# Kernel optimization log

Measured on AMD Instinct MI355X. Metric: run time of the kernel, lower is better.

The kernel has to match this reference:

```python
import math
import jax, jax.numpy as jnp
import numpy as np

S, D = 4096, 2048
H, DH = 16, 128
ROPE_BASE = 10000.0


def _rotate_half(x):
    # x: [..., dh]; pairs (x1, x2) -> (-x2, x1), interleaved
    shp = x.shape
    x = x.reshape(*shp[:-1], shp[-1] // 2, 2)
    x1, x2 = x[..., 0], x[..., 1]
    return jnp.stack((-x2, x1), axis=-1).reshape(shp)


def _rope_cos_sin(seq_len, dh):
    inv_freq = 1.0 / (ROPE_BASE ** (jnp.arange(0, dh, 2, dtype=jnp.float32) / dh))
    t = jnp.arange(seq_len, dtype=jnp.float32)
    freqs = jnp.einsum('i,j->ij', t, inv_freq)  # [S, dh/2]
    cos = jnp.repeat(jnp.cos(freqs), 2, axis=-1)  # [S, dh]
    sin = jnp.repeat(jnp.sin(freqs), 2, axis=-1)
    return cos, sin


def setup_inputs() -> dict:
    key = jax.random.key(0)
    kx, kq, kk, kv, ko = jax.random.split(key, 5)
    scale_in = 1.0 / math.sqrt(D)
    scale_hd = 1.0 / math.sqrt(H * DH)
    return {
        'x': jax.random.normal(kx, (S, D), dtype=jnp.float32),
        'mask': jnp.tril(jnp.ones((S, S), dtype=bool)),  # causal
        'wq': jax.random.normal(kq, (H * DH, D), dtype=jnp.float32) * scale_in,
        'wk': jax.random.normal(kk, (H * DH, D), dtype=jnp.float32) * scale_in,
        'wv': jax.random.normal(kv, (H * DH, D), dtype=jnp.float32) * scale_in,
        'wo': jax.random.normal(ko, (D, H * DH), dtype=jnp.float32) * scale_hd,
    }


def reference(x, mask, wq, wk, wv, wo):
    s = x.shape[0]
    # QKV projections (Linear: y = W @ x per token) -> [h, S, dh]
    q = (x @ wq.T).reshape(s, H, DH).transpose(1, 0, 2)
    k = (x @ wk.T).reshape(s, H, DH).transpose(1, 0, 2)
    v = (x @ wv.T).reshape(s, H, DH).transpose(1, 0, 2)
    # RoPE
    cos, sin = _rope_cos_sin(s, DH)  # [S, dh] each
    q = q * cos[None] + _rotate_half(q) * sin[None]
    k = k * cos[None] + _rotate_half(k) * sin[None]
    # Attention
    sim = jnp.einsum('hid,hjd->hij', q, k) / math.sqrt(DH)  # [h, S, S]
    sim = jnp.where(mask[None], sim, -jnp.inf)
    attn = jax.nn.softmax(sim, axis=-1)
    out = jnp.einsum('hij,hjd->ihd', attn, v).reshape(s, H * DH)
    return out @ wo.T
```

## Files before the change

kernel.cpp:

```cpp
#include <hip/hip_runtime.h>
#include <stdint.h>

#define S_LEN 4096
#define D_MODEL 2048
#define NH 16
#define DH 128

typedef short s16x8 __attribute__((ext_vector_type(8)));
typedef short s16x2 __attribute__((ext_vector_type(2)));
typedef unsigned short u16;
typedef unsigned short u16x4 __attribute__((ext_vector_type(4)));
typedef float f32x4 __attribute__((ext_vector_type(4)));

__device__ __forceinline__ u16 f2bf(float f) {
  union { float f; uint32_t u; } v; v.f = f;
  uint32_t u = v.u;
  u += 0x7FFFu + ((u >> 16) & 1u);
  return (u16)(u >> 16);
}

__device__ __forceinline__ float bf2f(u16 b) {
  union { uint32_t u; float f; } v; v.u = ((uint32_t)b) << 16;
  return v.f;
}

__device__ __forceinline__ void async_copy16(const u16* g, u16* l) {
  __builtin_amdgcn_global_load_lds(
      (const __attribute__((address_space(1))) unsigned int*)g,
      (__attribute__((address_space(3))) unsigned int*)l, 16, 0, 0);
}

__global__ void cast_kernel(const float4* __restrict__ src, u16* __restrict__ dst, int n4) {
  int i = blockIdx.x * blockDim.x + threadIdx.x;
  if (i >= n4) return;
  float4 v = src[i];
  u16x4 o;
  o[0] = f2bf(v.x); o[1] = f2bf(v.y); o[2] = f2bf(v.z); o[3] = f2bf(v.w);
  *(u16x4*)(dst + (size_t)i * 4) = o;
}

__global__ void cast4_kernel(const float4* __restrict__ s0, const float4* __restrict__ s1,
                             const float4* __restrict__ s2, const float4* __restrict__ s3,
                             u16* __restrict__ d0, u16* __restrict__ d1,
                             u16* __restrict__ d2, u16* __restrict__ d3) {
  int b = blockIdx.x;
  int which = b >> 12;
  const float4* src = which == 0 ? s0 : which == 1 ? s1 : which == 2 ? s2 : s3;
  u16* dst = which == 0 ? d0 : which == 1 ? d1 : which == 2 ? d2 : d3;
  int i = (b & 4095) * blockDim.x + threadIdx.x;
  float4 v = src[i];
  u16x4 o;
  o[0] = f2bf(v.x); o[1] = f2bf(v.y); o[2] = f2bf(v.z); o[3] = f2bf(v.w);
  *(u16x4*)(dst + (size_t)i * 4) = o;
}

__global__ void rope_table(float* __restrict__ ctab, float* __restrict__ stab) {
  int idx = blockIdx.x * blockDim.x + threadIdx.x;
  int t = idx >> 6, p = idx & 63;
  float invf = powf(10000.0f, -(float)p / 64.0f);
  float th = (float)t * invf;
  ctab[idx] = cosf(th);
  stab[idx] = sinf(th);
}

__global__ __launch_bounds__(256) void gemm_qkv(
    const u16* __restrict__ A,
    const u16* __restrict__ wqb, const u16* __restrict__ wkb, const u16* __restrict__ wvb,
    u16* __restrict__ qh, u16* __restrict__ kh, u16* __restrict__ vh,
    const float* __restrict__ ctab, const float* __restrict__ stab)
{
  __shared__ __align__(16) u16 la[128 * 64];
  __shared__ __align__(16) u16 lb[128 * 64];
  const int tid = threadIdx.x;
  const int w = tid >> 6, lane = tid & 63, quad = lane >> 4, l16 = lane & 15;
  const int wm = (w & 1) << 6, wn = (w >> 1) << 6;
  const int m0 = blockIdx.x << 7;
  const int n0g = blockIdx.y << 7;
  const int which = n0g >> 11;
  const int n0 = n0g & 2047;
  const u16* B = which == 0 ? wqb : which == 1 ? wkb : wvb;
  u16* outp = which == 0 ? qh : which == 1 ? kh : vh;
  const int K = D_MODEL;

  f32x4 zero = {0.f, 0.f, 0.f, 0.f};
  f32x4 acc[4][4];
#pragma unroll
  for (int i = 0; i < 4; ++i)
#pragma unroll
    for (int j = 0; j < 4; ++j) acc[i][j] = zero;

  for (int k0 = 0; k0 < K; k0 += 64) {
    __syncthreads();
#pragma unroll
    for (int rnd = 0; rnd < 4; ++rnd) {
      int c = rnd * 256 + w * 64 + lane;
      int r = c >> 3, cc = c & 7;
      int gcol = ((cc ^ (r & 7)) << 3);
      int base = (rnd * 256 + w * 64) << 3;
      async_copy16(A + (size_t)(m0 + r) * K + k0 + gcol, la + base);
      async_copy16(B + (size_t)(n0 + r) * K + k0 + gcol, lb + base);
    }
    __syncthreads();
#pragma unroll
    for (int ks = 0; ks < 2; ++ks) {
      s16x8 af[4], bfr[4];
#pragma unroll
      for (int t = 0; t < 4; ++t) {
        int rowa = wm + (t << 4) + l16;
        af[t] = *(const s16x8*)(la + (rowa << 6) + ((((ks << 2) + quad) ^ (rowa & 7)) << 3));
        int rowb = wn + (t << 4) + l16;
        bfr[t] = *(const s16x8*)(lb + (rowb << 6) + ((((ks << 2) + quad) ^ (rowb & 7)) << 3));
      }
#pragma unroll
      for (int mt = 0; mt < 4; ++mt)
#pragma unroll
        for (int nt = 0; nt < 4; ++nt)
          acc[mt][nt] = __builtin_amdgcn_mfma_f32_16x16x32_bf16(af[mt], bfr[nt], acc[mt][nt], 0, 0, 0);
    }
  }

#pragma unroll
  for (int mt = 0; mt < 4; ++mt) {
    int rowg = m0 + wm + (mt << 4) + (quad << 2);
#pragma unroll
    for (int nt = 0; nt < 4; ++nt) {
      int cl = n0 + wn + (nt << 4) + l16;
      int hh = cl >> 7, dd = cl & 127;
      int p = dd >> 1;
      f32x4 v = acc[mt][nt];
#pragma unroll
      for (int r = 0; r < 4; ++r) {
        float val = v[r];
        if (which < 2) {
          float partner = __shfl_xor(val, 1);
          float c = ctab[(size_t)(rowg + r) * 64 + p];
          float s = stab[(size_t)(rowg + r) * 64 + p];
          val = (dd & 1) ? fmaf(val, c, partner * s) : fmaf(val, c, -partner * s);
        }
        outp[((size_t)hh * S_LEN + (rowg + r)) * DH + dd] = f2bf(val);
      }
    }
  }
}

__global__ __launch_bounds__(256) void gemm_bf16(
    const u16* __restrict__ A, const u16* __restrict__ B,
    float* __restrict__ outF, int M, int N, int K)
{
  __shared__ __align__(16) u16 la[128 * 64];
  __shared__ __align__(16) u16 lb[128 * 64];
  const int tid = threadIdx.x;
  const int w = tid >> 6, lane = tid & 63, quad = lane >> 4, l16 = lane & 15;
  const int wm = (w & 1) << 6, wn = (w >> 1) << 6;
  const int m0 = blockIdx.x << 7, n0 = blockIdx.y << 7;

  f32x4 zero = {0.f, 0.f, 0.f, 0.f};
  f32x4 acc[4][4];
#pragma unroll
  for (int i = 0; i < 4; ++i)
#pragma unroll
    for (int j = 0; j < 4; ++j) acc[i][j] = zero;

  for (int k0 = 0; k0 < K; k0 += 64) {
    __syncthreads();
#pragma unroll
    for (int rnd = 0; rnd < 4; ++rnd) {
      int c = rnd * 256 + w * 64 + lane;
      int r = c >> 3, cc = c & 7;
      int gcol = ((cc ^ (r & 7)) << 3);
      int base = (rnd * 256 + w * 64) << 3;
      async_copy16(A + (size_t)(m0 + r) * K + k0 + gcol, la + base);
      async_copy16(B + (size_t)(n0 + r) * K + k0 + gcol, lb + base);
    }
    __syncthreads();
#pragma unroll
    for (int ks = 0; ks < 2; ++ks) {
      s16x8 af[4], bfr[4];
#pragma unroll
      for (int t = 0; t < 4; ++t) {
        int rowa = wm + (t << 4) + l16;
        af[t] = *(const s16x8*)(la + (rowa << 6) + ((((ks << 2) + quad) ^ (rowa & 7)) << 3));
        int rowb = wn + (t << 4) + l16;
        bfr[t] = *(const s16x8*)(lb + (rowb << 6) + ((((ks << 2) + quad) ^ (rowb & 7)) << 3));
      }
#pragma unroll
      for (int mt = 0; mt < 4; ++mt)
#pragma unroll
        for (int nt = 0; nt < 4; ++nt)
          acc[mt][nt] = __builtin_amdgcn_mfma_f32_16x16x32_bf16(af[mt], bfr[nt], acc[mt][nt], 0, 0, 0);
    }
  }

#pragma unroll
  for (int mt = 0; mt < 4; ++mt) {
    int rowg = m0 + wm + (mt << 4) + (quad << 2);
#pragma unroll
    for (int nt = 0; nt < 4; ++nt) {
      int col = n0 + wn + (nt << 4) + l16;
      f32x4 v = acc[mt][nt];
#pragma unroll
      for (int r = 0; r < 4; ++r) outF[(size_t)(rowg + r) * N + col] = v[r];
    }
  }
}

__global__ __launch_bounds__(512) void attn_kernel(
    const u16* __restrict__ Q, const u16* __restrict__ Kb,
    const u16* __restrict__ V,
    u16* __restrict__ U0, u16* __restrict__ U1, float* __restrict__ lbuf)
{
  __shared__ __align__(16) u16 lk[64 * 128];
  __shared__ __align__(16) u16 lvt[128 * 64];

  const int tid = threadIdx.x;
  const int w = tid >> 6, lane = tid & 63, quad = lane >> 4, l16 = lane & 15;
  const int h = blockIdx.y;
  const int bx = blockIdx.x;

  const u16* Qh = Q + (size_t)h * S_LEN * DH;
  const u16* Kh = Kb + (size_t)h * S_LEN * DH;
  const u16* Vh = V + (size_t)h * S_LEN * DH;

  const float scale = 0.08838834764831845f;
  const s16x8 vones = {0x3F80, 0x3F80, 0x3F80, 0x3F80, 0x3F80, 0x3F80, 0x3F80, 0x3F80};
  f32x4 zero = {0.f, 0.f, 0.f, 0.f};

  for (int seg = 0; seg < 2; ++seg) {
    const int qt = seg ? bx : (31 - bx);
    const int jlo = seg ? (qt + 1) : 0;
    const int jhi = seg ? (2 * qt + 2) : (qt + 1);
    const int i0 = qt << 7;
    const int iw = i0 + (w << 4);

    s16x8 qf[4];
#pragma unroll
    for (int ks = 0; ks < 4; ++ks)
      qf[ks] = *(const s16x8*)(Qh + (size_t)(iw + l16) * DH + ks * 32 + quad * 8);

    f32x4 accO[8];
#pragma unroll
    for (int dt = 0; dt < 8; ++dt) accO[dt] = zero;
    f32x4 accL = zero;

    for (int jt = jlo; jt < jhi; ++jt) {
      const int j0 = jt << 6;
      __syncthreads();
#pragma unroll
      for (int rnd = 0; rnd < 2; ++rnd) {
        int c = rnd * 512 + tid;
        int r = c >> 4, cc = c & 15;
        int gcol = ((cc ^ (r & 15)) << 3);
        async_copy16(Kh + (size_t)(j0 + r) * DH + gcol, lk + ((rnd * 512 + w * 64) << 3));
      }
      {
        int u = tid & 31;
        int c8 = tid >> 5;
        int r0 = u << 1;
        s16x8 v0 = *(const s16x8*)(Vh + (size_t)(j0 + r0) * DH + (c8 << 3));
        s16x8 v1 = *(const s16x8*)(Vh + (size_t)(j0 + r0 + 1) * DH + (c8 << 3));
        int cc = r0 >> 3;
#pragma unroll
        for (int e = 0; e < 8; ++e) {
          int d = (c8 << 3) + e;
          int off = (d << 6) + ((cc ^ (d & 7)) << 3) + (r0 & 7);
          s16x2 pr = {v0[e], v1[e]};
          *(s16x2*)(lvt + off) = pr;
        }
      }
      __syncthreads();

      f32x4 sa[4];
#pragma unroll
      for (int nt = 0; nt < 4; ++nt) sa[nt] = zero;
#pragma unroll
      for (int ks = 0; ks < 4; ++ks) {
#pragma unroll
        for (int nt = 0; nt < 4; ++nt) {
          int row = (nt << 4) + l16;
          s16x8 kf = *(const s16x8*)(lk + (row << 7) + ((((ks << 2) + quad) ^ (row & 15)) << 3));
          sa[nt] = __builtin_amdgcn_mfma_f32_16x16x32_bf16(qf[ks], kf, sa[nt], 0, 0, 0);
        }
      }

      __syncthreads();

      const bool maskt = (j0 + 63 > iw);
      u16* lpw = lk + (w << 10);
#pragma unroll
      for (int nt = 0; nt < 4; ++nt) {
        int col = (nt << 4) + l16;
        int j = j0 + col;
        int ccp = col >> 3;
#pragma unroll
        for (int r = 0; r < 4; ++r) {
          float raw = sa[nt][r];
          if (maskt) {
            int i = iw + (quad << 2) + r;
            if (j > i) raw = -1.0e30f;
          }
          float p = __expf(fmaf(raw, scale, -8.0f));
          union { float f; uint32_t u; } pv; pv.f = p;
          int m = (quad << 2) + r;
          lpw[(m << 6) + ((ccp ^ (m & 7)) << 3) + (col & 7)] = (u16)(pv.u >> 16);
        }
      }
      asm volatile("s_waitcnt lgkmcnt(0)" ::: "memory");
      s16x8 pf[2];
#pragma unroll
      for (int kp = 0; kp < 2; ++kp)
        pf[kp] = *(const s16x8*)(lpw + (l16 << 6) + ((((kp << 2) + quad) ^ (l16 & 7)) << 3));

      accL = __builtin_amdgcn_mfma_f32_16x16x32_bf16(pf[0], vones, accL, 0, 0, 0);
      accL = __builtin_amdgcn_mfma_f32_16x16x32_bf16(pf[1], vones, accL, 0, 0, 0);

#pragma unroll
      for (int dt = 0; dt < 8; ++dt) {
#pragma unroll
        for (int kp = 0; kp < 2; ++kp) {
          int row = (dt << 4) + l16;
          s16x8 vf = *(const s16x8*)(lvt + (row << 6) + ((((kp << 2) + quad) ^ (row & 7)) << 3));
          accO[dt] = __builtin_amdgcn_mfma_f32_16x16x32_bf16(pf[kp], vf, accO[dt], 0, 0, 0);
        }
      }
    }

    u16* Useg = seg ? U1 : U0;
    float* ls = lbuf + (size_t)seg * NH * S_LEN + (size_t)h * S_LEN;
#pragma unroll
    for (int r = 0; r < 4; ++r) {
      float lr = accL[r];
      float inv = lr > 0.f ? 1.0f / lr : 0.f;
      int srow = iw + (quad << 2) + r;
#pragma unroll
      for (int dt = 0; dt < 8; ++dt)
        Useg[((size_t)h * S_LEN + srow) * DH + (dt << 4) + l16] = f2bf(accO[dt][r] * inv);
      if (l16 == 0) ls[srow] = lr;
    }
  }
}

__global__ void combine_kernel(const u16* __restrict__ U0, const u16* __restrict__ U1,
                               const float* __restrict__ lbuf, u16* __restrict__ ob)
{
  int t = blockIdx.x * 256 + threadIdx.x;
  int d8 = t & 15;
  int h = (t >> 4) & 15;
  int s = t >> 8;
  float l0 = lbuf[(size_t)h * S_LEN + s];
  float l1 = lbuf[(size_t)(NH * S_LEN) + (size_t)h * S_LEN + s];
  float inv = 1.0f / (l0 + l1);
  float w0 = l0 * inv, w1 = l1 * inv;
  size_t base = ((size_t)h * S_LEN + s) * DH + d8 * 8;
  s16x8 u0 = *(const s16x8*)(U0 + base);
  s16x8 u1 = *(const s16x8*)(U1 + base);
  u16 o[8];
#pragma unroll
  for (int e = 0; e < 8; ++e)
    o[e] = f2bf(w0 * bf2f((u16)u0[e]) + w1 * bf2f((u16)u1[e]));
  *(s16x8*)(ob + ((size_t)s * D_MODEL + h * DH + d8 * 8)) = *(s16x8*)o;
}

extern "C" void kernel_launch(void* const* d_in, const int* in_sizes, int n_in,
                              void* d_out, int out_size, void* d_ws, size_t ws_size,
                              hipStream_t stream) {
  const float* x  = (const float*)d_in[0];
  const float* wq = (const float*)d_in[2];
  const float* wk = (const float*)d_in[3];
  const float* wv = (const float*)d_in[4];
  const float* wo = (const float*)d_in[5];
  float* out = (float*)d_out;

  char* ws = (char*)d_ws;
  u16* xb  = (u16*)(ws);
  u16* wqb = (u16*)(ws + (16ull << 20));
  u16* wkb = (u16*)(ws + (24ull << 20));
  u16* wvb = (u16*)(ws + (32ull << 20));
  u16* wob = (u16*)(ws + (40ull << 20));
  u16* qh  = (u16*)(ws + (48ull << 20));
  u16* kh  = (u16*)(ws + (64ull << 20));
  u16* vh  = (u16*)(ws + (80ull << 20));
  float* ctab = (float*)(ws + (96ull << 20));
  float* stab = (float*)(ws + (97ull << 20));
  u16* U0 = (u16*)(ws);
  u16* U1 = (u16*)(ws + (16ull << 20));
  float* lbuf = (float*)(ws + (32ull << 20));
  u16* ob = qh;

  const int nx4 = S_LEN * D_MODEL / 4;
  cast_kernel<<<nx4 / 256, 256, 0, stream>>>((const float4*)x, xb, nx4);
  cast4_kernel<<<4 * 4096, 256, 0, stream>>>(
      (const float4*)wq, (const float4*)wk, (const float4*)wv, (const float4*)wo,
      wqb, wkb, wvb, wob);
  rope_table<<<(S_LEN * 64) / 256, 256, 0, stream>>>(ctab, stab);

  gemm_qkv<<<dim3(S_LEN / 128, 3 * D_MODEL / 128), 256, 0, stream>>>(
      xb, wqb, wkb, wvb, qh, kh, vh, ctab, stab);

  attn_kernel<<<dim3(32, NH), 512, 0, stream>>>(qh, kh, vh, U0, U1, lbuf);
  combine_kernel<<<S_LEN * NH * 16 / 256, 256, 0, stream>>>(U0, U1, lbuf, ob);

  gemm_bf16<<<dim3(S_LEN / 128, D_MODEL / 128), 256, 0, stream>>>(
      ob, wob, out, S_LEN, D_MODEL, D_MODEL);
}
```

Baseline: 526.5 us.

## Double-buffer K/V tiles in attention kernel and prefetch next tile during compute

Splits the K and transposed-V shared tiles into two buffers and gives P its own shared region. The next tile's K is issued as an async copy and its V loaded into registers while the current tile's QK and PV MFMAs run, and the V transpose store goes into the alternate buffer. This cuts the per-iteration barriers from three to one. It also wraps the MFMA sections in s_setprio. The cost is more LDS per block (about 80KB) and more registers, which can lower occupancy.

```diff
diff --git a/kernel.cpp b/kernel.cpp
--- a/kernel.cpp
+++ b/kernel.cpp
@@ -209,8 +209,9 @@
     const u16* __restrict__ V,
     u16* __restrict__ U0, u16* __restrict__ U1, float* __restrict__ lbuf)
 {
-  __shared__ __align__(16) u16 lk[64 * 128];
-  __shared__ __align__(16) u16 lvt[128 * 64];
+  __shared__ __align__(16) u16 lk[2][64 * 128];
+  __shared__ __align__(16) u16 lvt[2][128 * 64];
+  __shared__ __align__(16) u16 lp[8 * 1024];
 
   const int tid = threadIdx.x;
   const int w = tid >> 6, lane = tid & 63, quad = lane >> 4, l16 = lane & 15;
@@ -224,6 +225,7 @@
   const float scale = 0.08838834764831845f;
   const s16x8 vones = {0x3F80, 0x3F80, 0x3F80, 0x3F80, 0x3F80, 0x3F80, 0x3F80, 0x3F80};
   f32x4 zero = {0.f, 0.f, 0.f, 0.f};
+  u16* lpw = lp + (w << 10);
 
   for (int seg = 0; seg < 2; ++seg) {
     const int qt = seg ? bx : (31 - bx);
@@ -242,50 +244,67 @@
     for (int dt = 0; dt < 8; ++dt) accO[dt] = zero;
     f32x4 accL = zero;
 
-    for (int jt = jlo; jt < jhi; ++jt) {
-      const int j0 = jt << 6;
-      __syncthreads();
+    {
+      const int j0 = jlo << 6;
+      int u = tid & 31, c8 = tid >> 5, r0 = u << 1;
+      s16x8 v0 = *(const s16x8*)(Vh + (size_t)(j0 + r0) * DH + (c8 << 3));
+      s16x8 v1 = *(const s16x8*)(Vh + (size_t)(j0 + r0 + 1) * DH + (c8 << 3));
 #pragma unroll
       for (int rnd = 0; rnd < 2; ++rnd) {
         int c = rnd * 512 + tid;
         int r = c >> 4, cc = c & 15;
         int gcol = ((cc ^ (r & 15)) << 3);
-        async_copy16(Kh + (size_t)(j0 + r) * DH + gcol, lk + ((rnd * 512 + w * 64) << 3));
-      }
-      {
-        int u = tid & 31;
-        int c8 = tid >> 5;
-        int r0 = u << 1;
-        s16x8 v0 = *(const s16x8*)(Vh + (size_t)(j0 + r0) * DH + (c8 << 3));
-        s16x8 v1 = *(const s16x8*)(Vh + (size_t)(j0 + r0 + 1) * DH + (c8 << 3));
-        int cc = r0 >> 3;
-#pragma unroll
-        for (int e = 0; e < 8; ++e) {
-          int d = (c8 << 3) + e;
-          int off = (d << 6) + ((cc ^ (d & 7)) << 3) + (r0 & 7);
-          s16x2 pr = {v0[e], v1[e]};
-          *(s16x2*)(lvt + off) = pr;
-        }
-      }
-      __syncthreads();
-
+        async_copy16(Kh + (size_t)(j0 + r) * DH + gcol, lk[0] + ((rnd * 512 + w * 64) << 3));
+      }
+      int cc = r0 >> 3;
+#pragma unroll
+      for (int e = 0; e < 8; ++e) {
+        int d = (c8 << 3) + e;
+        int off = (d << 6) + ((cc ^ (d & 7)) << 3) + (r0 & 7);
+        s16x2 pr = {v0[e], v1[e]};
+        *(s16x2*)(lvt[0] + off) = pr;
+      }
+    }
+    __syncthreads();
+
+    int cur = 0;
+    for (int jt = jlo; jt < jhi; ++jt) {
+      const int j0 = jt << 6;
+      const bool has_next = (jt + 1) < jhi;
+
+      s16x8 nv0, nv1;
+      if (has_next) {
+        const int nj0 = (jt + 1) << 6;
+        int u = tid & 31, c8 = tid >> 5, r0 = u << 1;
+        nv0 = *(const s16x8*)(Vh + (size_t)(nj0 + r0) * DH + (c8 << 3));
+        nv1 = *(const s16x8*)(Vh + (size_t)(nj0 + r0 + 1) * DH + (c8 << 3));
+#pragma unroll
+        for (int rnd = 0; rnd < 2; ++rnd) {
+          int c = rnd * 512 + tid;
+          int r = c >> 4, cc = c & 15;
+          int gcol = ((cc ^ (r & 15)) << 3);
+          async_copy16(Kh + (size_t)(nj0 + r) * DH + gcol,
+                       lk[cur ^ 1] + ((rnd * 512 + w * 64) << 3));
+        }
+      }
+
+      const u16* lkc = lk[cur];
       f32x4 sa[4];
 #pragma unroll
       for (int nt = 0; nt < 4; ++nt) sa[nt] = zero;
+      __builtin_amdgcn_s_setprio(1);
 #pragma unroll
       for (int ks = 0; ks < 4; ++ks) {
 #pragma unroll
         for (int nt = 0; nt < 4; ++nt) {
           int row = (nt << 4) + l16;
-          s16x8 kf = *(const s16x8*)(lk + (row << 7) + ((((ks << 2) + quad) ^ (row & 15)) << 3));
+          s16x8 kf = *(const s16x8*)(lkc + (row << 7) + ((((ks << 2) + quad) ^ (row & 15)) << 3));
           sa[nt] = __builtin_amdgcn_mfma_f32_16x16x32_bf16(qf[ks], kf, sa[nt], 0, 0, 0);
         }
       }
-
-      __syncthreads();
+      __builtin_amdgcn_s_setprio(0);
 
       const bool maskt = (j0 + 63 > iw);
-      u16* lpw = lk + (w << 10);
 #pragma unroll
       for (int nt = 0; nt < 4; ++nt) {
         int col = (nt << 4) + l16;
@@ -310,18 +329,36 @@
       for (int kp = 0; kp < 2; ++kp)
         pf[kp] = *(const s16x8*)(lpw + (l16 << 6) + ((((kp << 2) + quad) ^ (l16 & 7)) << 3));
 
+      if (has_next) {
+        int u = tid & 31, c8 = tid >> 5, r0 = u << 1;
+        int cc = r0 >> 3;
+        u16* dst = lvt[cur ^ 1];
+#pragma unroll
+        for (int e = 0; e < 8; ++e) {
+          int d = (c8 << 3) + e;
+          int off = (d << 6) + ((cc ^ (d & 7)) << 3) + (r0 & 7);
+          s16x2 pr = {nv0[e], nv1[e]};
+          *(s16x2*)(dst + off) = pr;
+        }
+      }
+
+      const u16* lvc = lvt[cur];
+      __builtin_amdgcn_s_setprio(1);
       accL = __builtin_amdgcn_mfma_f32_16x16x32_bf16(pf[0], vones, accL, 0, 0, 0);
       accL = __builtin_amdgcn_mfma_f32_16x16x32_bf16(pf[1], vones, accL, 0, 0, 0);
-
 #pragma unroll
       for (int dt = 0; dt < 8; ++dt) {
 #pragma unroll
         for (int kp = 0; kp < 2; ++kp) {
           int row = (dt << 4) + l16;
-          s16x8 vf = *(const s16x8*)(lvt + (row << 6) + ((((kp << 2) + quad) ^ (row & 7)) << 3));
+          s16x8 vf = *(const s16x8*)(lvc + (row << 6) + ((((kp << 2) + quad) ^ (row & 7)) << 3));
           accO[dt] = __builtin_amdgcn_mfma_f32_16x16x32_bf16(pf[kp], vf, accO[dt], 0, 0, 0);
         }
       }
+      __builtin_amdgcn_s_setprio(0);
+
+      __syncthreads();
+      cur ^= 1;
     }
 
     u16* Useg = seg ? U1 : U0;
```

Result: faster. 510.7 us (-3.0%).
